# Kernel optimization log

Measured on AMD Instinct MI355X. Metric: run time of the kernel, lower is better.

The kernel has to match this reference:

```python
import jax, jax.numpy as jnp
import numpy as np

SLACKNESS_PENALTY = 1.0
WEIGHT_DECAY = 1e-5

POS_LEN, NUM_NEG = 32768, 64
N_RULES, N_UNLABEL = 262144, 131072
NUM_ENT, NUM_REL, EMB_DIM = 100000, 500, 256


def _rand_triples(key, n):
    k1, k2, k3 = jax.random.split(key, 3)
    h = jax.random.randint(k1, (n,), 0, NUM_ENT)
    r = jax.random.randint(k2, (n,), 0, NUM_REL)
    t = jax.random.randint(k3, (n,), 0, NUM_ENT)
    return jnp.stack([h, r, t], axis=1)  # [n, 3]


def setup_inputs() -> dict:
    key = jax.random.key(0)
    ks = jax.random.split(key, 10)
    pos_score = jax.random.normal(ks[0], (POS_LEN, 1), dtype=jnp.float32)
    neg_score = jax.random.normal(ks[1], (POS_LEN, NUM_NEG), dtype=jnp.float32)
    confidence = jax.random.uniform(ks[2], (N_RULES,), dtype=jnp.float32)
    ent_emb = jax.random.normal(ks[3], (NUM_ENT, EMB_DIM), dtype=jnp.float32) * 0.1
    rel_emb = jax.random.normal(ks[4], (NUM_REL, EMB_DIM), dtype=jnp.float32) * 0.1
    rule_p1 = _rand_triples(ks[5], N_RULES)
    rule_p2 = _rand_triples(ks[6], N_RULES)
    triple_num = jax.random.randint(ks[7], (N_RULES,), 2, 4)  # values in {2, 3}
    unlabel_ids = jax.random.randint(ks[8], (N_RULES,), 0, N_UNLABEL)
    unlabel_triples = _rand_triples(ks[9], N_UNLABEL)
    return dict(pos_score=pos_score, neg_score=neg_score, confidence=confidence,
                ent_emb=ent_emb, rel_emb=rel_emb, rule_p1=rule_p1, rule_p2=rule_p2,
                triple_num=triple_num, unlabel_ids=unlabel_ids,
                unlabel_triples=unlabel_triples)


def _score(triples, ent_emb, rel_emb):
    # DistMult KGE score: sum_d e_h * w_r * e_t  -> [n, 1]
    h = ent_emb[triples[:, 0]]
    r = rel_emb[triples[:, 1]]
    t = ent_emb[triples[:, 2]]
    return jnp.sum(h * r * t, axis=-1, keepdims=True)


def reference(pos_score, neg_score, confidence, ent_emb, rel_emb,
              rule_p1, rule_p2, triple_num, unlabel_ids, unlabel_triples):
    # BCE(sigmoid(pos), 1) = softplus(-x); BCE(sigmoid(neg), 0) = softplus(x)
    positive_loss = jnp.mean(jax.nn.softplus(-pos_score))
    negative_loss = jnp.mean(jax.nn.softplus(neg_score))

    # Per-rule body sigmoids (originally memoized one-row model() calls)
    s1 = jax.nn.sigmoid(_score(rule_p1, ent_emb, rel_emb))[:, 0]  # [n_rules]
    s2 = jax.nn.sigmoid(_score(rule_p2, ent_emb, rel_emb))[:, 0]
    contrib = SLACKNESS_PENALTY * confidence * s1 * jnp.where(triple_num == 3, s2, 1.0)
    # pi_gradient dict scatter-add -> segment_sum over unique unlabel triples
    pi_grad = jax.ops.segment_sum(contrib, unlabel_ids,
                                  num_segments=unlabel_triples.shape[0])  # [n_unlabel]

    su = _score(unlabel_triples, ent_emb, rel_emb)  # [n_unlabel, 1]
    p = jax.nn.sigmoid(su)
    # target = clip(p + pi_grad, 0, 1), detached (original uses .cpu().detach().numpy())
    tgt = jax.lax.stop_gradient(jnp.clip(p + pi_grad[:, None], 0.0, 1.0))
    # BCE(p, tgt) with stable log-sigmoid forms
    unlabel_loss = jnp.mean(tgt * jax.nn.softplus(-su) + (1.0 - tgt) * jax.nn.softplus(su))

    regularization = WEIGHT_DECAY * (jnp.sum(ent_emb ** 2) + jnp.sum(rel_emb ** 2))
    return positive_loss + negative_loss + unlabel_loss + regularization
```

## Files before the change

### kernel.cpp

```cpp
#include <hip/hip_runtime.h>
#include <cstddef>
#include <cstdint>

#define POS_LEN    32768
#define NUM_NEG    64
#define N_RULES    262144
#define N_UNLABEL  131072
#define NUM_ENT    100000
#define NUM_REL    500
#define EMB_DIM    256
#define WEIGHT_DECAY 1e-5

#define AUX_BLOCKS    2048
#define GATHER_BLOCKS 2048
#define LOSS_BLOCKS   1024

typedef __attribute__((ext_vector_type(2))) float        f32x2;
typedef __attribute__((ext_vector_type(4))) float        f32x4;
typedef __attribute__((ext_vector_type(2))) unsigned int u32x2;
typedef __attribute__((ext_vector_type(4))) unsigned int u32x4;

__device__ __forceinline__ float softplusf_(float x) {
    return fmaxf(x, 0.0f) + log1pf(expf(-fabsf(x)));
}
__device__ __forceinline__ float sigmoidf_(float x) {
    return 1.0f / (1.0f + expf(-x));
}
__device__ __forceinline__ float quarter_sum16(float v) {
#pragma unroll
    for (int m = 1; m <= 8; m <<= 1) v += __shfl_xor(v, m, 64);
    return v;
}
__device__ __forceinline__ float wave_sum64(float v) {
#pragma unroll
    for (int m = 32; m >= 1; m >>= 1) v += __shfl_xor(v, m, 64);
    return v;
}
__device__ __forceinline__ double wave_sum64d(double v) {
#pragma unroll
    for (int m = 32; m >= 1; m >>= 1) v += __shfl_xor(v, m, 64);
    return v;
}

__device__ __forceinline__ u32x2 f32x8_to_fp8(const f32x4 a, const f32x4 b) {
    int lo = 0, hi = 0;
    lo = __builtin_amdgcn_cvt_pk_fp8_f32(a[0], a[1], lo, false);
    lo = __builtin_amdgcn_cvt_pk_fp8_f32(a[2], a[3], lo, true);
    hi = __builtin_amdgcn_cvt_pk_fp8_f32(b[0], b[1], hi, false);
    hi = __builtin_amdgcn_cvt_pk_fp8_f32(b[2], b[3], hi, true);
    u32x2 r; r[0] = (unsigned)lo; r[1] = (unsigned)hi; return r;
}

__device__ __forceinline__ float dot3_q(const u32x4 hv, const u32x4 rv, const u32x4 tv) {
    f32x2 acc = {0.0f, 0.0f};
#pragma unroll
    for (int w = 0; w < 4; ++w) {
        f32x2 h0 = __builtin_amdgcn_cvt_pk_f32_fp8((int)hv[w], false);
        f32x2 h1 = __builtin_amdgcn_cvt_pk_f32_fp8((int)hv[w], true);
        f32x2 r0 = __builtin_amdgcn_cvt_pk_f32_fp8((int)rv[w], false);
        f32x2 r1 = __builtin_amdgcn_cvt_pk_f32_fp8((int)rv[w], true);
        f32x2 t0 = __builtin_amdgcn_cvt_pk_f32_fp8((int)tv[w], false);
        f32x2 t1 = __builtin_amdgcn_cvt_pk_f32_fp8((int)tv[w], true);
        acc += (h0 * r0) * t0;
        acc += (h1 * r1) * t1;
    }
    return quarter_sum16(acc[0] + acc[1]);
}

__global__ __launch_bounds__(256) void aux_fp8_kernel(const float* __restrict__ ent,
                                                      const float* __restrict__ rel,
                                                      u32x2* __restrict__ ent8,
                                                      u32x2* __restrict__ rel8,
                                                      float* __restrict__ pi_grad,
                                                      float* __restrict__ auxp) {
    const int tid = blockIdx.x * blockDim.x + threadIdx.x;
    const int stride = gridDim.x * blockDim.x;
    for (int i = tid; i < N_UNLABEL; i += stride) pi_grad[i] = 0.0f;

    float sq = 0.0f;
    const f32x4* entv = reinterpret_cast<const f32x4*>(ent);
    for (int i = tid; i < (NUM_ENT * EMB_DIM) / 8; i += stride) {
        f32x4 a = __builtin_nontemporal_load(entv + (size_t)i * 2);
        f32x4 b = __builtin_nontemporal_load(entv + (size_t)i * 2 + 1);
        sq += a[0]*a[0] + a[1]*a[1] + a[2]*a[2] + a[3]*a[3]
            + b[0]*b[0] + b[1]*b[1] + b[2]*b[2] + b[3]*b[3];
        ent8[i] = f32x8_to_fp8(a, b);
    }
    const f32x4* relv = reinterpret_cast<const f32x4*>(rel);
    for (int i = tid; i < (NUM_REL * EMB_DIM) / 8; i += stride) {
        f32x4 a = __builtin_nontemporal_load(relv + (size_t)i * 2);
        f32x4 b = __builtin_nontemporal_load(relv + (size_t)i * 2 + 1);
        sq += a[0]*a[0] + a[1]*a[1] + a[2]*a[2] + a[3]*a[3]
            + b[0]*b[0] + b[1]*b[1] + b[2]*b[2] + b[3]*b[3];
        rel8[i] = f32x8_to_fp8(a, b);
    }
    sq = wave_sum64(sq);
    __shared__ float ls[8];
    const int lane = threadIdx.x & 63, wid = threadIdx.x >> 6;
    if (lane == 0) ls[wid] = sq;
    __syncthreads();
    if (threadIdx.x == 0) {
        float bs = 0.0f;
        for (int w = 0; w < (int)(blockDim.x >> 6); ++w) bs += ls[w];
        auxp[blockIdx.x] = bs;
    }
}

__global__ void gather_kernel(const float* __restrict__ conf,
                              const u32x4* __restrict__ ent8,
                              const u32x4* __restrict__ rel8,
                              const int* __restrict__ p1,
                              const int* __restrict__ p2,
                              const int* __restrict__ tnum,
                              const int* __restrict__ uids,
                              const int* __restrict__ ut,
                              float* __restrict__ pi_grad,
                              float* __restrict__ su_out) {
    const int lane = threadIdx.x & 63;
    const int l    = lane & 15;
    const int q    = lane >> 4;
    const int wave  = blockIdx.x * (blockDim.x >> 6) + (threadIdx.x >> 6);
    const int nwave = gridDim.x * (blockDim.x >> 6);
    const int nr4 = N_RULES / 4, nu4 = N_UNLABEL / 4;

    for (int pi = wave; pi < nr4; pi += 2 * nwave) {
        const int pj = pi + nwave;
        const int ruleA = pi * 4 + q;
        const int ruleB = pj * 4 + q;
        const int ba = ruleA * 3, bb = ruleB * 3;
        const int hA1 = p1[ba], rA1 = p1[ba + 1], tA1 = p1[ba + 2];
        const int hB1 = p1[bb], rB1 = p1[bb + 1], tB1 = p1[bb + 2];
        const bool has2A = (tnum[ruleA] == 3);
        const bool has2B = (tnum[ruleB] == 3);
        const float cfA = conf[ruleA], cfB = conf[ruleB];
        const int uidA = uids[ruleA], uidB = uids[ruleB];
        const u32x4 HA1 = ent8[(size_t)hA1 * 16 + l];
        const u32x4 RA1 = rel8[(size_t)rA1 * 16 + l];
        const u32x4 TA1 = ent8[(size_t)tA1 * 16 + l];
        const u32x4 HB1 = ent8[(size_t)hB1 * 16 + l];
        const u32x4 RB1 = rel8[(size_t)rB1 * 16 + l];
        const u32x4 TB1 = ent8[(size_t)tB1 * 16 + l];
        u32x4 HA2 = {0,0,0,0}, RA2 = {0,0,0,0}, TA2 = {0,0,0,0};
        if (has2A) {
            HA2 = ent8[(size_t)p2[ba] * 16 + l];
            RA2 = rel8[(size_t)p2[ba + 1] * 16 + l];
            TA2 = ent8[(size_t)p2[ba + 2] * 16 + l];
        }
        u32x4 HB2 = {0,0,0,0}, RB2 = {0,0,0,0}, TB2 = {0,0,0,0};
        if (has2B) {
            HB2 = ent8[(size_t)p2[bb] * 16 + l];
            RB2 = rel8[(size_t)p2[bb + 1] * 16 + l];
            TB2 = ent8[(size_t)p2[bb + 2] * 16 + l];
        }
        float cA = sigmoidf_(dot3_q(HA1, RA1, TA1)) * cfA;
        if (has2A) cA *= sigmoidf_(dot3_q(HA2, RA2, TA2));
        float cB = sigmoidf_(dot3_q(HB1, RB1, TB1)) * cfB;
        if (has2B) cB *= sigmoidf_(dot3_q(HB2, RB2, TB2));
        if (l == 0) {
            atomicAdd(&pi_grad[uidA], cA);
            atomicAdd(&pi_grad[uidB], cB);
        }
    }

    for (int pi = wave; pi < nu4; pi += 2 * nwave) {
        const int i0 = pi * 4 + q;
        const int i1 = (pi + nwave) * 4 + q;
        const int b0 = i0 * 3, b1 = i1 * 3;
        const int h0 = ut[b0], r0 = ut[b0 + 1], t0 = ut[b0 + 2];
        const int h1 = ut[b1], r1 = ut[b1 + 1], t1 = ut[b1 + 2];
        const u32x4 H0 = ent8[(size_t)h0 * 16 + l];
        const u32x4 R0 = rel8[(size_t)r0 * 16 + l];
        const u32x4 T0 = ent8[(size_t)t0 * 16 + l];
        const u32x4 H1 = ent8[(size_t)h1 * 16 + l];
        const u32x4 R1 = rel8[(size_t)r1 * 16 + l];
        const u32x4 T1 = ent8[(size_t)t1 * 16 + l];
        const float s0 = dot3_q(H0, R0, T0);
        const float s1 = dot3_q(H1, R1, T1);
        if (l == 0) {
            su_out[i0] = s0;
            su_out[i1] = s1;
        }
    }
}

__global__ __launch_bounds__(256) void loss_kernel(const float* __restrict__ su,
                                                   const float* __restrict__ pi_grad,
                                                   const float* __restrict__ pos,
                                                   const float* __restrict__ neg,
                                                   float* __restrict__ lossp) {
    const int tid = blockIdx.x * blockDim.x + threadIdx.x;
    const int stride = gridDim.x * blockDim.x;
    float ul = 0.0f, ps = 0.0f, ns = 0.0f;
    for (int i = tid; i < N_UNLABEL; i += stride) {
        const float s   = su[i];
        const float p   = sigmoidf_(s);
        const float tgt = fminf(fmaxf(p + pi_grad[i], 0.0f), 1.0f);
        ul += tgt * softplusf_(-s) + (1.0f - tgt) * softplusf_(s);
    }
    const f32x4* posv = reinterpret_cast<const f32x4*>(pos);
    for (int i = tid; i < POS_LEN / 4; i += stride) {
        f32x4 v = __builtin_nontemporal_load(posv + i);
        ps += softplusf_(-v[0]) + softplusf_(-v[1]) + softplusf_(-v[2]) + softplusf_(-v[3]);
    }
    const f32x4* negv = reinterpret_cast<const f32x4*>(neg);
    for (int i = tid; i < (POS_LEN * NUM_NEG) / 4; i += stride) {
        f32x4 v = __builtin_nontemporal_load(negv + i);
        ns += softplusf_(v[0]) + softplusf_(v[1]) + softplusf_(v[2]) + softplusf_(v[3]);
    }
    ul = wave_sum64(ul); ps = wave_sum64(ps); ns = wave_sum64(ns);
    __shared__ float lu[8], lp[8], ln[8];
    const int lane = threadIdx.x & 63, wid = threadIdx.x >> 6;
    if (lane == 0) { lu[wid] = ul; lp[wid] = ps; ln[wid] = ns; }
    __syncthreads();
    if (threadIdx.x == 0) {
        float bu = 0.0f, bp = 0.0f, bn = 0.0f;
        for (int w = 0; w < (int)(blockDim.x >> 6); ++w) { bu += lu[w]; bp += lp[w]; bn += ln[w]; }
        lossp[blockIdx.x]                   = bu;
        lossp[LOSS_BLOCKS + blockIdx.x]     = bp;
        lossp[2 * LOSS_BLOCKS + blockIdx.x] = bn;
    }
}

__global__ void finalize_kernel(const float* __restrict__ auxp,
                                const float* __restrict__ lossp,
                                float* __restrict__ out) {
    const int lane = threadIdx.x;
    double sq = 0.0, ul = 0.0, ps = 0.0, ns = 0.0;
    for (int i = lane; i < AUX_BLOCKS; i += 64) sq += (double)auxp[i];
    for (int i = lane; i < LOSS_BLOCKS; i += 64) {
        ul += (double)lossp[i];
        ps += (double)lossp[LOSS_BLOCKS + i];
        ns += (double)lossp[2 * LOSS_BLOCKS + i];
    }
    sq = wave_sum64d(sq); ul = wave_sum64d(ul);
    ps = wave_sum64d(ps); ns = wave_sum64d(ns);
    if (lane == 0) {
        double v = ps / (double)POS_LEN
                 + ns / ((double)POS_LEN * (double)NUM_NEG)
                 + ul / (double)N_UNLABEL
                 + WEIGHT_DECAY * sq;
        out[0] = (float)v;
    }
}

extern "C" void kernel_launch(void* const* d_in, const int* in_sizes, int n_in,
                              void* d_out, int out_size, void* d_ws, size_t ws_size,
                              hipStream_t stream) {
    const float* pos  = (const float*)d_in[0];
    const float* neg  = (const float*)d_in[1];
    const float* conf = (const float*)d_in[2];
    const float* ent  = (const float*)d_in[3];
    const float* rel  = (const float*)d_in[4];
    const int*   p1   = (const int*)d_in[5];
    const int*   p2   = (const int*)d_in[6];
    const int*   tnum = (const int*)d_in[7];
    const int*   uids = (const int*)d_in[8];
    const int*   ut   = (const int*)d_in[9];

    const size_t off_pi    = 0;
    const size_t off_su    = off_pi + (size_t)N_UNLABEL * 4;
    const size_t off_auxp  = off_su + (size_t)N_UNLABEL * 4;
    const size_t off_lossp = off_auxp + (size_t)AUX_BLOCKS * 4;
    const size_t off_tab   = (off_lossp + (size_t)3 * LOSS_BLOCKS * 4 + 511) & ~(size_t)511;
    const size_t off_rel8  = off_tab + (size_t)NUM_ENT * EMB_DIM;

    float* pi_grad = (float*)((char*)d_ws + off_pi);
    float* su      = (float*)((char*)d_ws + off_su);
    float* auxp    = (float*)((char*)d_ws + off_auxp);
    float* lossp   = (float*)((char*)d_ws + off_lossp);
    u32x2* ent8w   = (u32x2*)((char*)d_ws + off_tab);
    u32x2* rel8w   = (u32x2*)((char*)d_ws + off_rel8);

    aux_fp8_kernel<<<AUX_BLOCKS, 256, 0, stream>>>(ent, rel, ent8w, rel8w, pi_grad, auxp);
    gather_kernel<<<GATHER_BLOCKS, 256, 0, stream>>>(conf,
                                                     (const u32x4*)((char*)d_ws + off_tab),
                                                     (const u32x4*)((char*)d_ws + off_rel8),
                                                     p1, p2, tnum, uids, ut, pi_grad, su);
    loss_kernel<<<LOSS_BLOCKS, 256, 0, stream>>>(su, pi_grad, pos, neg, lossp);
    finalize_kernel<<<1, 64, 0, stream>>>(auxp, lossp, (float*)d_out);
}
```

Measured before the change: 96.05 us.

## Partition rules by triple count into compacted lists to remove divergent gathers

```diff
diff --git a/kernel.cpp b/kernel.cpp
--- a/kernel.cpp
+++ b/kernel.cpp
@@ -69,34 +69,70 @@
 
 __global__ __launch_bounds__(256) void aux_fp8_kernel(const float* __restrict__ ent,
                                                       const float* __restrict__ rel,
-                                                      u32x2* __restrict__ ent8,
-                                                      u32x2* __restrict__ rel8,
+                                                      u32x4* __restrict__ ent8,
+                                                      u32x4* __restrict__ rel8,
+                                                      const int* __restrict__ tnum,
+                                                      int* __restrict__ list2,
+                                                      int* __restrict__ list3,
+                                                      unsigned* __restrict__ cnts,
                                                       float* __restrict__ pi_grad,
                                                       float* __restrict__ auxp) {
     const int tid = blockIdx.x * blockDim.x + threadIdx.x;
     const int stride = gridDim.x * blockDim.x;
+    const int lane = threadIdx.x & 63, wid = threadIdx.x >> 6;
+
     for (int i = tid; i < N_UNLABEL; i += stride) pi_grad[i] = 0.0f;
+
+    for (int rule = tid; rule < N_RULES; rule += stride) {
+        const bool has2 = (tnum[rule] == 3);
+        const unsigned long long m3 = __ballot(has2);
+        const unsigned long long m2 = ~m3;
+        const unsigned long long below = (lane == 63) ? ~0ull >> 1
+                                         : ((1ull << lane) - 1ull) | 0ull;
+        unsigned base3 = 0, base2 = 0;
+        if (lane == 0) {
+            base3 = atomicAdd(&cnts[1], (unsigned)__popcll(m3));
+            base2 = atomicAdd(&cnts[0], (unsigned)__popcll(m2));
+        }
+        base3 = __shfl(base3, 0);
+        base2 = __shfl(base2, 0);
+        if (has2) list3[base3 + __popcll(m3 & below)] = rule;
+        else      list2[base2 + __popcll(m2 & below)] = rule;
+    }
 
     float sq = 0.0f;
     const f32x4* entv = reinterpret_cast<const f32x4*>(ent);
-    for (int i = tid; i < (NUM_ENT * EMB_DIM) / 8; i += stride) {
-        f32x4 a = __builtin_nontemporal_load(entv + (size_t)i * 2);
-        f32x4 b = __builtin_nontemporal_load(entv + (size_t)i * 2 + 1);
+    for (int i = tid; i < (NUM_ENT * EMB_DIM) / 16; i += stride) {
+        f32x4 a = __builtin_nontemporal_load(entv + (size_t)i * 4);
+        f32x4 b = __builtin_nontemporal_load(entv + (size_t)i * 4 + 1);
+        f32x4 c = __builtin_nontemporal_load(entv + (size_t)i * 4 + 2);
+        f32x4 d = __builtin_nontemporal_load(entv + (size_t)i * 4 + 3);
         sq += a[0]*a[0] + a[1]*a[1] + a[2]*a[2] + a[3]*a[3]
-            + b[0]*b[0] + b[1]*b[1] + b[2]*b[2] + b[3]*b[3];
-        ent8[i] = f32x8_to_fp8(a, b);
+            + b[0]*b[0] + b[1]*b[1] + b[2]*b[2] + b[3]*b[3]
+            + c[0]*c[0] + c[1]*c[1] + c[2]*c[2] + c[3]*c[3]
+            + d[0]*d[0] + d[1]*d[1] + d[2]*d[2] + d[3]*d[3];
+        u32x2 lo = f32x8_to_fp8(a, b);
+        u32x2 hi = f32x8_to_fp8(c, d);
+        u32x4 o; o[0] = lo[0]; o[1] = lo[1]; o[2] = hi[0]; o[3] = hi[1];
+        ent8[i] = o;
     }
     const f32x4* relv = reinterpret_cast<const f32x4*>(rel);
-    for (int i = tid; i < (NUM_REL * EMB_DIM) / 8; i += stride) {
-        f32x4 a = __builtin_nontemporal_load(relv + (size_t)i * 2);
-        f32x4 b = __builtin_nontemporal_load(relv + (size_t)i * 2 + 1);
+    for (int i = tid; i < (NUM_REL * EMB_DIM) / 16; i += stride) {
+        f32x4 a = __builtin_nontemporal_load(relv + (size_t)i * 4);
+        f32x4 b = __builtin_nontemporal_load(relv + (size_t)i * 4 + 1);
+        f32x4 c = __builtin_nontemporal_load(relv + (size_t)i * 4 + 2);
+        f32x4 d = __builtin_nontemporal_load(relv + (size_t)i * 4 + 3);
         sq += a[0]*a[0] + a[1]*a[1] + a[2]*a[2] + a[3]*a[3]
-            + b[0]*b[0] + b[1]*b[1] + b[2]*b[2] + b[3]*b[3];
-        rel8[i] = f32x8_to_fp8(a, b);
+            + b[0]*b[0] + b[1]*b[1] + b[2]*b[2] + b[3]*b[3]
+            + c[0]*c[0] + c[1]*c[1] + c[2]*c[2] + c[3]*c[3]
+            + d[0]*d[0] + d[1]*d[1] + d[2]*d[2] + d[3]*d[3];
+        u32x2 lo = f32x8_to_fp8(a, b);
+        u32x2 hi = f32x8_to_fp8(c, d);
+        u32x4 o; o[0] = lo[0]; o[1] = lo[1]; o[2] = hi[0]; o[3] = hi[1];
+        rel8[i] = o;
     }
     sq = wave_sum64(sq);
     __shared__ float ls[8];
-    const int lane = threadIdx.x & 63, wid = threadIdx.x >> 6;
     if (lane == 0) ls[wid] = sq;
     __syncthreads();
     if (threadIdx.x == 0) {
@@ -111,9 +147,11 @@
                               const u32x4* __restrict__ rel8,
                               const int* __restrict__ p1,
                               const int* __restrict__ p2,
-                              const int* __restrict__ tnum,
                               const int* __restrict__ uids,
                               const int* __restrict__ ut,
+                              const int* __restrict__ list2,
+                              const int* __restrict__ list3,
+                              const unsigned* __restrict__ cnts,
                               float* __restrict__ pi_grad,
                               float* __restrict__ su_out) {
     const int lane = threadIdx.x & 63;
@@ -121,47 +159,57 @@
     const int q    = lane >> 4;
     const int wave  = blockIdx.x * (blockDim.x >> 6) + (threadIdx.x >> 6);
     const int nwave = gridDim.x * (blockDim.x >> 6);
-    const int nr4 = N_RULES / 4, nu4 = N_UNLABEL / 4;
-
-    for (int pi = wave; pi < nr4; pi += 2 * nwave) {
-        const int pj = pi + nwave;
-        const int ruleA = pi * 4 + q;
-        const int ruleB = pj * 4 + q;
+    const int n2 = (int)cnts[0];
+    const int n3 = (int)cnts[1];
+
+    const int it2 = (n2 + 3) >> 2;
+    for (int k = wave; k < it2; k += 2 * nwave) {
+        const int kB = k + nwave;
+        const int iA = k * 4 + q;
+        const int iB = kB * 4 + q;
+        const bool vA = iA < n2;
+        const bool vB = (kB < it2) && (iB < n2);
+        const int ruleA = vA ? list2[iA] : 0;
+        const int ruleB = vB ? list2[iB] : 0;
         const int ba = ruleA * 3, bb = ruleB * 3;
-        const int hA1 = p1[ba], rA1 = p1[ba + 1], tA1 = p1[ba + 2];
-        const int hB1 = p1[bb], rB1 = p1[bb + 1], tB1 = p1[bb + 2];
-        const bool has2A = (tnum[ruleA] == 3);
-        const bool has2B = (tnum[ruleB] == 3);
+        const int hA = p1[ba], rA = p1[ba + 1], tA = p1[ba + 2];
+        const int hB = p1[bb], rB = p1[bb + 1], tB = p1[bb + 2];
         const float cfA = conf[ruleA], cfB = conf[ruleB];
         const int uidA = uids[ruleA], uidB = uids[ruleB];
-        const u32x4 HA1 = ent8[(size_t)hA1 * 16 + l];
-        const u32x4 RA1 = rel8[(size_t)rA1 * 16 + l];
-        const u32x4 TA1 = ent8[(size_t)tA1 * 16 + l];
-        const u32x4 HB1 = ent8[(size_t)hB1 * 16 + l];
-        const u32x4 RB1 = rel8[(size_t)rB1 * 16 + l];
-        const u32x4 TB1 = ent8[(size_t)tB1 * 16 + l];
-        u32x4 HA2 = {0,0,0,0}, RA2 = {0,0,0,0}, TA2 = {0,0,0,0};
-        if (has2A) {
-            HA2 = ent8[(size_t)p2[ba] * 16 + l];
-            RA2 = rel8[(size_t)p2[ba + 1] * 16 + l];
-            TA2 = ent8[(size_t)p2[ba + 2] * 16 + l];
-        }
-        u32x4 HB2 = {0,0,0,0}, RB2 = {0,0,0,0}, TB2 = {0,0,0,0};
-        if (has2B) {
-            HB2 = ent8[(size_t)p2[bb] * 16 + l];
-            RB2 = rel8[(size_t)p2[bb + 1] * 16 + l];
-            TB2 = ent8[(size_t)p2[bb + 2] * 16 + l];
-        }
-        float cA = sigmoidf_(dot3_q(HA1, RA1, TA1)) * cfA;
-        if (has2A) cA *= sigmoidf_(dot3_q(HA2, RA2, TA2));
-        float cB = sigmoidf_(dot3_q(HB1, RB1, TB1)) * cfB;
-        if (has2B) cB *= sigmoidf_(dot3_q(HB2, RB2, TB2));
-        if (l == 0) {
-            atomicAdd(&pi_grad[uidA], cA);
-            atomicAdd(&pi_grad[uidB], cB);
-        }
-    }
-
+        const u32x4 HA = ent8[(size_t)hA * 16 + l];
+        const u32x4 RA = rel8[(size_t)rA * 16 + l];
+        const u32x4 TA = ent8[(size_t)tA * 16 + l];
+        const u32x4 HB = ent8[(size_t)hB * 16 + l];
+        const u32x4 RB = rel8[(size_t)rB * 16 + l];
+        const u32x4 TB = ent8[(size_t)tB * 16 + l];
+        const float cA = sigmoidf_(dot3_q(HA, RA, TA)) * cfA;
+        const float cB = sigmoidf_(dot3_q(HB, RB, TB)) * cfB;
+        if (l == 0 && vA) atomicAdd(&pi_grad[uidA], cA);
+        if (l == 0 && vB) atomicAdd(&pi_grad[uidB], cB);
+    }
+
+    const int it3 = (n3 + 3) >> 2;
+    for (int k = wave; k < it3; k += nwave) {
+        const int i = k * 4 + q;
+        const bool v = i < n3;
+        const int rule = v ? list3[i] : 0;
+        const int b = rule * 3;
+        const int h1 = p1[b], r1 = p1[b + 1], t1 = p1[b + 2];
+        const int h2 = p2[b], r2 = p2[b + 1], t2 = p2[b + 2];
+        const float cf = conf[rule];
+        const int uid = uids[rule];
+        const u32x4 H1 = ent8[(size_t)h1 * 16 + l];
+        const u32x4 R1 = rel8[(size_t)r1 * 16 + l];
+        const u32x4 T1 = ent8[(size_t)t1 * 16 + l];
+        const u32x4 H2 = ent8[(size_t)h2 * 16 + l];
+        const u32x4 R2 = rel8[(size_t)r2 * 16 + l];
+        const u32x4 T2 = ent8[(size_t)t2 * 16 + l];
+        float c = sigmoidf_(dot3_q(H1, R1, T1)) * cf
+                * sigmoidf_(dot3_q(H2, R2, T2));
+        if (l == 0 && v) atomicAdd(&pi_grad[uid], c);
+    }
+
+    const int nu4 = N_UNLABEL / 4;
     for (int pi = wave; pi < nu4; pi += 2 * nwave) {
         const int i0 = pi * 4 + q;
         const int i1 = (pi + nwave) * 4 + q;
@@ -171,11 +219,11 @@
         const u32x4 H0 = ent8[(size_t)h0 * 16 + l];
         const u32x4 R0 = rel8[(size_t)r0 * 16 + l];
         const u32x4 T0 = ent8[(size_t)t0 * 16 + l];
-        const u32x4 H1 = ent8[(size_t)h1 * 16 + l];
-        const u32x4 R1 = rel8[(size_t)r1 * 16 + l];
-        const u32x4 T1 = ent8[(size_t)t1 * 16 + l];
+        const u32x4 H1v = ent8[(size_t)h1 * 16 + l];
+        const u32x4 R1v = rel8[(size_t)r1 * 16 + l];
+        const u32x4 T1v = ent8[(size_t)t1 * 16 + l];
         const float s0 = dot3_q(H0, R0, T0);
-        const float s1 = dot3_q(H1, R1, T1);
+        const float s1 = dot3_q(H1v, R1v, T1v);
         if (l == 0) {
             su_out[i0] = s0;
             su_out[i1] = s1;
@@ -261,21 +309,27 @@
     const size_t off_su    = off_pi + (size_t)N_UNLABEL * 4;
     const size_t off_auxp  = off_su + (size_t)N_UNLABEL * 4;
     const size_t off_lossp = off_auxp + (size_t)AUX_BLOCKS * 4;
-    const size_t off_tab   = (off_lossp + (size_t)3 * LOSS_BLOCKS * 4 + 511) & ~(size_t)511;
+    const size_t off_cnts  = off_lossp + (size_t)3 * LOSS_BLOCKS * 4;
+    const size_t off_l2    = (off_cnts + 8 + 255) & ~(size_t)255;
+    const size_t off_l3    = off_l2 + (size_t)N_RULES * 4;
+    const size_t off_tab   = (off_l3 + (size_t)N_RULES * 4 + 511) & ~(size_t)511;
     const size_t off_rel8  = off_tab + (size_t)NUM_ENT * EMB_DIM;
 
-    float* pi_grad = (float*)((char*)d_ws + off_pi);
-    float* su      = (float*)((char*)d_ws + off_su);
-    float* auxp    = (float*)((char*)d_ws + off_auxp);
-    float* lossp   = (float*)((char*)d_ws + off_lossp);
-    u32x2* ent8w   = (u32x2*)((char*)d_ws + off_tab);
-    u32x2* rel8w   = (u32x2*)((char*)d_ws + off_rel8);
-
-    aux_fp8_kernel<<<AUX_BLOCKS, 256, 0, stream>>>(ent, rel, ent8w, rel8w, pi_grad, auxp);
-    gather_kernel<<<GATHER_BLOCKS, 256, 0, stream>>>(conf,
-                                                     (const u32x4*)((char*)d_ws + off_tab),
-                                                     (const u32x4*)((char*)d_ws + off_rel8),
-                                                     p1, p2, tnum, uids, ut, pi_grad, su);
+    float*    pi_grad = (float*)((char*)d_ws + off_pi);
+    float*    su      = (float*)((char*)d_ws + off_su);
+    float*    auxp    = (float*)((char*)d_ws + off_auxp);
+    float*    lossp   = (float*)((char*)d_ws + off_lossp);
+    unsigned* cnts    = (unsigned*)((char*)d_ws + off_cnts);
+    int*      list2   = (int*)((char*)d_ws + off_l2);
+    int*      list3   = (int*)((char*)d_ws + off_l3);
+    u32x4*    ent8    = (u32x4*)((char*)d_ws + off_tab);
+    u32x4*    rel8    = (u32x4*)((char*)d_ws + off_rel8);
+
+    hipMemsetAsync(cnts, 0, 8, stream);
+    aux_fp8_kernel<<<AUX_BLOCKS, 256, 0, stream>>>(ent, rel, ent8, rel8, tnum,
+                                                   list2, list3, cnts, pi_grad, auxp);
+    gather_kernel<<<GATHER_BLOCKS, 256, 0, stream>>>(conf, ent8, rel8, p1, p2, uids, ut,
+                                                     list2, list3, cnts, pi_grad, su);
     loss_kernel<<<LOSS_BLOCKS, 256, 0, stream>>>(su, pi_grad, pos, neg, lossp);
     finalize_kernel<<<1, 64, 0, stream>>>(auxp, lossp, (float*)d_out);
 }
```

Measured after the change: 205.7 us. 114% more time.

## Fuse unlabeled triple scoring into loss kernel, dropping intermediate score buffer

Applied to the files above, without the earlier changes.

```diff
diff --git a/kernel.cpp b/kernel.cpp
--- a/kernel.cpp
+++ b/kernel.cpp
@@ -12,8 +12,8 @@
 #define WEIGHT_DECAY 1e-5
 
 #define AUX_BLOCKS    2048
-#define GATHER_BLOCKS 2048
-#define LOSS_BLOCKS   1024
+#define RULE_BLOCKS   2048
+#define UL_BLOCKS     2048
 
 typedef __attribute__((ext_vector_type(2))) float        f32x2;
 typedef __attribute__((ext_vector_type(4))) float        f32x4;
@@ -106,22 +106,20 @@
     }
 }
 
-__global__ void gather_kernel(const float* __restrict__ conf,
-                              const u32x4* __restrict__ ent8,
-                              const u32x4* __restrict__ rel8,
-                              const int* __restrict__ p1,
-                              const int* __restrict__ p2,
-                              const int* __restrict__ tnum,
-                              const int* __restrict__ uids,
-                              const int* __restrict__ ut,
-                              float* __restrict__ pi_grad,
-                              float* __restrict__ su_out) {
+__global__ void rules_kernel(const float* __restrict__ conf,
+                             const u32x4* __restrict__ ent8,
+                             const u32x4* __restrict__ rel8,
+                             const int* __restrict__ p1,
+                             const int* __restrict__ p2,
+                             const int* __restrict__ tnum,
+                             const int* __restrict__ uids,
+                             float* __restrict__ pi_grad) {
     const int lane = threadIdx.x & 63;
     const int l    = lane & 15;
     const int q    = lane >> 4;
     const int wave  = blockIdx.x * (blockDim.x >> 6) + (threadIdx.x >> 6);
     const int nwave = gridDim.x * (blockDim.x >> 6);
-    const int nr4 = N_RULES / 4, nu4 = N_UNLABEL / 4;
+    const int nr4 = N_RULES / 4;
 
     for (int pi = wave; pi < nr4; pi += 2 * nwave) {
         const int pj = pi + nwave;
@@ -161,42 +159,63 @@
             atomicAdd(&pi_grad[uidB], cB);
         }
     }
-
-    for (int pi = wave; pi < nu4; pi += 2 * nwave) {
-        const int i0 = pi * 4 + q;
-        const int i1 = (pi + nwave) * 4 + q;
-        const int b0 = i0 * 3, b1 = i1 * 3;
+}
+
+__global__ void unlabel_loss_kernel(const u32x4* __restrict__ ent8,
+                                    const u32x4* __restrict__ rel8,
+                                    const int* __restrict__ ut,
+                                    const float* __restrict__ pi_grad,
+                                    const float* __restrict__ pos,
+                                    const float* __restrict__ neg,
+                                    float* __restrict__ ulossp) {
+    const int lane = threadIdx.x & 63;
+    const int l    = lane & 15;
+    const int q    = lane >> 4;
+    const int wave  = blockIdx.x * (blockDim.x >> 6) + (threadIdx.x >> 6);
+    const int nwave = gridDim.x * (blockDim.x >> 6);
+    const int tid = blockIdx.x * blockDim.x + threadIdx.x;
+    const int stride = gridDim.x * blockDim.x;
+
+    float ul = 0.0f;
+    {
+        const int i0 = (wave + 0 * nwave) * 4 + q;
+        const int i1 = (wave + 1 * nwave) * 4 + q;
+        const int i2 = (wave + 2 * nwave) * 4 + q;
+        const int i3 = (wave + 3 * nwave) * 4 + q;
+        const int b0 = i0 * 3, b1 = i1 * 3, b2 = i2 * 3, b3 = i3 * 3;
         const int h0 = ut[b0], r0 = ut[b0 + 1], t0 = ut[b0 + 2];
         const int h1 = ut[b1], r1 = ut[b1 + 1], t1 = ut[b1 + 2];
+        const int h2 = ut[b2], r2 = ut[b2 + 1], t2 = ut[b2 + 2];
+        const int h3 = ut[b3], r3 = ut[b3 + 1], t3 = ut[b3 + 2];
         const u32x4 H0 = ent8[(size_t)h0 * 16 + l];
         const u32x4 R0 = rel8[(size_t)r0 * 16 + l];
         const u32x4 T0 = ent8[(size_t)t0 * 16 + l];
         const u32x4 H1 = ent8[(size_t)h1 * 16 + l];
         const u32x4 R1 = rel8[(size_t)r1 * 16 + l];
         const u32x4 T1 = ent8[(size_t)t1 * 16 + l];
+        const u32x4 H2 = ent8[(size_t)h2 * 16 + l];
+        const u32x4 R2 = rel8[(size_t)r2 * 16 + l];
+        const u32x4 T2 = ent8[(size_t)t2 * 16 + l];
+        const u32x4 H3 = ent8[(size_t)h3 * 16 + l];
+        const u32x4 R3 = rel8[(size_t)r3 * 16 + l];
+        const u32x4 T3 = ent8[(size_t)t3 * 16 + l];
         const float s0 = dot3_q(H0, R0, T0);
         const float s1 = dot3_q(H1, R1, T1);
+        const float s2 = dot3_q(H2, R2, T2);
+        const float s3 = dot3_q(H3, R3, T3);
         if (l == 0) {
-            su_out[i0] = s0;
-            su_out[i1] = s1;
+            float tg0 = fminf(fmaxf(sigmoidf_(s0) + pi_grad[i0], 0.0f), 1.0f);
+            float tg1 = fminf(fmaxf(sigmoidf_(s1) + pi_grad[i1], 0.0f), 1.0f);
+            float tg2 = fminf(fmaxf(sigmoidf_(s2) + pi_grad[i2], 0.0f), 1.0f);
+            float tg3 = fminf(fmaxf(sigmoidf_(s3) + pi_grad[i3], 0.0f), 1.0f);
+            ul += tg0 * softplusf_(-s0) + (1.0f - tg0) * softplusf_(s0);
+            ul += tg1 * softplusf_(-s1) + (1.0f - tg1) * softplusf_(s1);
+            ul += tg2 * softplusf_(-s2) + (1.0f - tg2) * softplusf_(s2);
+            ul += tg3 * softplusf_(-s3) + (1.0f - tg3) * softplusf_(s3);
         }
     }
-}
-
-__global__ __launch_bounds__(256) void loss_kernel(const float* __restrict__ su,
-                                                   const float* __restrict__ pi_grad,
-                                                   const float* __restrict__ pos,
-                                                   const float* __restrict__ neg,
-                                                   float* __restrict__ lossp) {
-    const int tid = blockIdx.x * blockDim.x + threadIdx.x;
-    const int stride = gridDim.x * blockDim.x;
-    float ul = 0.0f, ps = 0.0f, ns = 0.0f;
-    for (int i = tid; i < N_UNLABEL; i += stride) {
-        const float s   = su[i];
-        const float p   = sigmoidf_(s);
-        const float tgt = fminf(fmaxf(p + pi_grad[i], 0.0f), 1.0f);
-        ul += tgt * softplusf_(-s) + (1.0f - tgt) * softplusf_(s);
-    }
+
+    float ps = 0.0f, ns = 0.0f;
     const f32x4* posv = reinterpret_cast<const f32x4*>(pos);
     for (int i = tid; i < POS_LEN / 4; i += stride) {
         f32x4 v = __builtin_nontemporal_load(posv + i);
@@ -207,30 +226,31 @@
         f32x4 v = __builtin_nontemporal_load(negv + i);
         ns += softplusf_(v[0]) + softplusf_(v[1]) + softplusf_(v[2]) + softplusf_(v[3]);
     }
+
     ul = wave_sum64(ul); ps = wave_sum64(ps); ns = wave_sum64(ns);
     __shared__ float lu[8], lp[8], ln[8];
-    const int lane = threadIdx.x & 63, wid = threadIdx.x >> 6;
+    const int wid = threadIdx.x >> 6;
     if (lane == 0) { lu[wid] = ul; lp[wid] = ps; ln[wid] = ns; }
     __syncthreads();
     if (threadIdx.x == 0) {
         float bu = 0.0f, bp = 0.0f, bn = 0.0f;
         for (int w = 0; w < (int)(blockDim.x >> 6); ++w) { bu += lu[w]; bp += lp[w]; bn += ln[w]; }
-        lossp[blockIdx.x]                   = bu;
-        lossp[LOSS_BLOCKS + blockIdx.x]     = bp;
-        lossp[2 * LOSS_BLOCKS + blockIdx.x] = bn;
+        ulossp[blockIdx.x]                 = bu;
+        ulossp[UL_BLOCKS + blockIdx.x]     = bp;
+        ulossp[2 * UL_BLOCKS + blockIdx.x] = bn;
     }
 }
 
 __global__ void finalize_kernel(const float* __restrict__ auxp,
-                                const float* __restrict__ lossp,
+                                const float* __restrict__ ulossp,
                                 float* __restrict__ out) {
     const int lane = threadIdx.x;
     double sq = 0.0, ul = 0.0, ps = 0.0, ns = 0.0;
     for (int i = lane; i < AUX_BLOCKS; i += 64) sq += (double)auxp[i];
-    for (int i = lane; i < LOSS_BLOCKS; i += 64) {
-        ul += (double)lossp[i];
-        ps += (double)lossp[LOSS_BLOCKS + i];
-        ns += (double)lossp[2 * LOSS_BLOCKS + i];
+    for (int i = lane; i < UL_BLOCKS; i += 64) {
+        ul += (double)ulossp[i];
+        ps += (double)ulossp[UL_BLOCKS + i];
+        ns += (double)ulossp[2 * UL_BLOCKS + i];
     }
     sq = wave_sum64d(sq); ul = wave_sum64d(ul);
     ps = wave_sum64d(ps); ns = wave_sum64d(ns);
@@ -258,24 +278,24 @@
     const int*   ut   = (const int*)d_in[9];
 
     const size_t off_pi    = 0;
-    const size_t off_su    = off_pi + (size_t)N_UNLABEL * 4;
-    const size_t off_auxp  = off_su + (size_t)N_UNLABEL * 4;
-    const size_t off_lossp = off_auxp + (size_t)AUX_BLOCKS * 4;
-    const size_t off_tab   = (off_lossp + (size_t)3 * LOSS_BLOCKS * 4 + 511) & ~(size_t)511;
+    const size_t off_auxp  = off_pi + (size_t)N_UNLABEL * 4;
+    const size_t off_ulp   = off_auxp + (size_t)AUX_BLOCKS * 4;
+    const size_t off_tab   = (off_ulp + (size_t)3 * UL_BLOCKS * 4 + 511) & ~(size_t)511;
     const size_t off_rel8  = off_tab + (size_t)NUM_ENT * EMB_DIM;
 
     float* pi_grad = (float*)((char*)d_ws + off_pi);
-    float* su      = (float*)((char*)d_ws + off_su);
     float* auxp    = (float*)((char*)d_ws + off_auxp);
-    float* lossp   = (float*)((char*)d_ws + off_lossp);
+    float* ulossp  = (float*)((char*)d_ws + off_ulp);
     u32x2* ent8w   = (u32x2*)((char*)d_ws + off_tab);
     u32x2* rel8w   = (u32x2*)((char*)d_ws + off_rel8);
 
     aux_fp8_kernel<<<AUX_BLOCKS, 256, 0, stream>>>(ent, rel, ent8w, rel8w, pi_grad, auxp);
-    gather_kernel<<<GATHER_BLOCKS, 256, 0, stream>>>(conf,
-                                                     (const u32x4*)((char*)d_ws + off_tab),
-                                                     (const u32x4*)((char*)d_ws + off_rel8),
-                                                     p1, p2, tnum, uids, ut, pi_grad, su);
-    loss_kernel<<<LOSS_BLOCKS, 256, 0, stream>>>(su, pi_grad, pos, neg, lossp);
-    finalize_kernel<<<1, 64, 0, stream>>>(auxp, lossp, (float*)d_out);
-}
+    rules_kernel<<<RULE_BLOCKS, 256, 0, stream>>>(conf,
+                                                  (const u32x4*)((char*)d_ws + off_tab),
+                                                  (const u32x4*)((char*)d_ws + off_rel8),
+                                                  p1, p2, tnum, uids, pi_grad);
+    unlabel_loss_kernel<<<UL_BLOCKS, 256, 0, stream>>>((const u32x4*)((char*)d_ws + off_tab),
+                                                       (const u32x4*)((char*)d_ws + off_rel8),
+                                                       ut, pi_grad, pos, neg, ulossp);
+    finalize_kernel<<<1, 64, 0, stream>>>(auxp, ulossp, (float*)d_out);
+}
```

Measured after the change: 108.8 us. 1.13x slower.
